# Kernel optimization log

Measured on AMD Instinct MI355X. Metric: run time of the kernel, lower is better.

The kernel has to match this reference:

```python
import jax, jax.numpy as jnp
import numpy as np

B, S, D_IN = 4, 2048, 1024
EMBED, HEADS = 1024, 16
HEAD_DIM = EMBED // HEADS


def setup_inputs() -> dict:
    key = jax.random.key(0)
    k1, k2, k3 = jax.random.split(key, 3)
    x = jax.random.normal(k1, (B, S, D_IN), dtype=jnp.float32)
    # xavier-uniform-ish init scales
    lim_qkv = float(np.sqrt(6.0 / (D_IN + 3 * EMBED)))
    lim_o = float(np.sqrt(6.0 / (EMBED + EMBED)))
    w_qkv = jax.random.uniform(k2, (3 * EMBED, D_IN), minval=-lim_qkv, maxval=lim_qkv, dtype=jnp.float32)
    b_qkv = jnp.zeros((3 * EMBED,), dtype=jnp.float32)
    w_o = jax.random.uniform(k3, (EMBED, EMBED), minval=-lim_o, maxval=lim_o, dtype=jnp.float32)
    b_o = jnp.zeros((EMBED,), dtype=jnp.float32)
    return {"x": x, "w_qkv": w_qkv, "b_qkv": b_qkv, "w_o": w_o, "b_o": b_o}


def reference(x, w_qkv, b_qkv, w_o, b_o):
    b, s, _ = x.shape
    qkv = jnp.einsum('bsi,oi->bso', x, w_qkv) + b_qkv            # (b, s, 3E)
    qkv = qkv.reshape(b, s, HEADS, 3 * HEAD_DIM).transpose(0, 2, 1, 3)  # (b, h, s, 3d)
    q, k, v = jnp.split(qkv, 3, axis=-1)                          # each (b, h, s, d)
    scale = 1.0 / jnp.sqrt(jnp.float32(HEAD_DIM))
    attn = jnp.einsum('bhqd,bhkd->bhqk', q, k) * scale            # (b, h, s, s)
    attn = jax.nn.softmax(attn, axis=-1)
    vals = jnp.einsum('bhqk,bhkd->bhqd', attn, v)                 # (b, h, s, d)
    # NOTE: original torch code reshapes (b,h,s,d) -> (b,s,e) WITHOUT transposing
    # heads back; jnp.reshape reproduces that flattening exactly.
    vals = vals.reshape(b, s, EMBED)
    out = jnp.einsum('bse,oe->bso', vals, w_o) + b_o              # (b, s, E)
    return out
```

## Files before the change

kernel.cpp:

```cpp
#include <hip/hip_runtime.h>
#include <stdint.h>
#include <stddef.h>

#define DEVINL __device__ __forceinline__

typedef unsigned short u16;
typedef unsigned int u32;
typedef __attribute__((ext_vector_type(8))) short short8;
typedef __attribute__((ext_vector_type(4))) float f32x4;
typedef __attribute__((ext_vector_type(4))) u32 u32x4;
typedef __attribute__((ext_vector_type(2))) u32 u32x2;

#define QSCALE 0.18033688011112042f

DEVINL u16 f2bf(float f) {
    u32 u = __builtin_bit_cast(u32, f);
    u32 r = (u + 0x7fffu + ((u >> 16) & 1u)) >> 16;
    return (u16)r;
}

DEVINL void gld_lds16(const void* g, void* l) {
    __builtin_amdgcn_global_load_lds(
        (__attribute__((address_space(1))) u32*)(uintptr_t)g,
        (__attribute__((address_space(3))) u32*)l, 16, 0, 0);
}

DEVINL u32 pack_bf16_trunc(float lo, float hi) {
    return __builtin_amdgcn_perm(__builtin_bit_cast(u32, hi),
                                 __builtin_bit_cast(u32, lo), 0x07060302u);
}

DEVINL void plswap32(u32 &a, u32 &b) {
#if __has_builtin(__builtin_amdgcn_permlane32_swap)
    u32x2 r = __builtin_amdgcn_permlane32_swap(a, b, false, false);
    a = r[0]; b = r[1];
#else
    asm("v_permlane32_swap_b32 %0, %1" : "+v"(a), "+v"(b));
#endif
}
DEVINL void plswap16(u32 &a, u32 &b) {
#if __has_builtin(__builtin_amdgcn_permlane16_swap)
    u32x2 r = __builtin_amdgcn_permlane16_swap(a, b, false, false);
    a = r[0]; b = r[1];
#else
    asm("v_permlane16_swap_b32 %0, %1" : "+v"(a), "+v"(b));
#endif
}

__global__ void prep_inputs(const float* __restrict__ x, const float* __restrict__ wqkv,
                            const float* __restrict__ bqkv, const float* __restrict__ wo,
                            u16* __restrict__ xb, u16* __restrict__ wqb,
                            u16* __restrict__ wob, float* __restrict__ bsc) {
    int blk = blockIdx.x;
    if (blk < 6144) {
        const float* src; u16* dst; int base; bool qscale = false;
        if (blk < 4096)      { src = x;    dst = xb;  base = blk; }
        else if (blk < 5632) { src = wqkv; dst = wqb; base = blk - 4096; qscale = true; }
        else                 { src = wo;   dst = wob; base = blk - 5632; }
        int i = (base * 256 + threadIdx.x) * 8;
        float sc = 1.0f;
        if (qscale) { int row = i >> 10; if ((row % 192) < 64) sc = QSCALE; }
        float4 a = *(const float4*)(src + i);
        float4 c = *(const float4*)(src + i + 4);
        union { u16 s[8]; u32x4 v; } t;
        t.s[0] = f2bf(a.x * sc); t.s[1] = f2bf(a.y * sc); t.s[2] = f2bf(a.z * sc); t.s[3] = f2bf(a.w * sc);
        t.s[4] = f2bf(c.x * sc); t.s[5] = f2bf(c.y * sc); t.s[6] = f2bf(c.z * sc); t.s[7] = f2bf(c.w * sc);
        *(u32x4*)(dst + i) = t.v;
    } else {
        int i = (blk - 6144) * 256 + threadIdx.x;
        float sc = ((i % 192) < 64) ? QSCALE : 1.0f;
        bsc[i] = bqkv[i] * sc;
    }
}

__global__ void gemm_qkv(const u16* __restrict__ A, const u16* __restrict__ Bm,
                         const float* __restrict__ bias, u16* __restrict__ qkvb,
                         u16* __restrict__ vtb) {
    const int K = 1024, N = 3072;
    __shared__ u16 As[128 * 32];
    __shared__ u16 Bs[128 * 32];
    const int tid = threadIdx.x;
    const int lane = tid & 63;
    const int wv = tid >> 6, wr = wv >> 1, wc = wv & 1;
    const int l15 = lane & 15, quad = lane >> 4;
    const int m0 = blockIdx.y * 128, n0 = blockIdx.x * 128;

    f32x4 acc[4][4];
#pragma unroll
    for (int i = 0; i < 4; i++)
#pragma unroll
        for (int j = 0; j < 4; j++) acc[i][j] = (f32x4){0.f, 0.f, 0.f, 0.f};

    const u16* Ab = A + (size_t)m0 * K;
    const u16* Bb = Bm + (size_t)n0 * K;
    const int srow = tid >> 2;
    const int sc8 = (tid & 3) * 8;

    for (int k0 = 0; k0 < K; k0 += 32) {
#pragma unroll
        for (int i = 0; i < 2; i++) {
            int row = i * 64 + srow;
            gld_lds16(Ab + (size_t)row * K + k0 + sc8, (char*)As + (size_t)(i * 256 + tid) * 16);
            gld_lds16(Bb + (size_t)row * K + k0 + sc8, (char*)Bs + (size_t)(i * 256 + tid) * 16);
        }
        __syncthreads();
        short8 af[4], bf8[4];
#pragma unroll
        for (int mi = 0; mi < 4; mi++)
            af[mi] = *(const short8*)(As + (wr * 64 + mi * 16 + l15) * 32 + quad * 8);
#pragma unroll
        for (int ni = 0; ni < 4; ni++)
            bf8[ni] = *(const short8*)(Bs + (wc * 64 + ni * 16 + l15) * 32 + quad * 8);
#pragma unroll
        for (int mi = 0; mi < 4; mi++)
#pragma unroll
            for (int ni = 0; ni < 4; ni++)
                acc[mi][ni] = __builtin_amdgcn_mfma_f32_16x16x32_bf16(af[mi], bf8[ni], acc[mi][ni], 0, 0, 0);
        __syncthreads();
    }

#pragma unroll
    for (int mi = 0; mi < 4; mi++) {
        int row_b = m0 + wr * 64 + mi * 16 + quad * 4;
#pragma unroll
        for (int ni = 0; ni < 4; ni++) {
            int c0 = n0 + wc * 64 + ni * 16;
            int sec0 = c0 % 192;
            float bv = bias[c0 + l15];
            float v0 = acc[mi][ni][0] + bv;
            float v1 = acc[mi][ni][1] + bv;
            float v2 = acc[mi][ni][2] + bv;
            float v3 = acc[mi][ni][3] + bv;
            if (sec0 >= 128) {
                int hh = c0 / 192;
                int b = row_b >> 11;
                int s = row_b & 2047;
                int d = sec0 - 128 + l15;
                u32 lo = (u32)f2bf(v0) | ((u32)f2bf(v1) << 16);
                u32 hi = (u32)f2bf(v2) | ((u32)f2bf(v3) << 16);
                *(u32x2*)(vtb + ((size_t)((b * 16 + hh) * 64 + d)) * 2048 + s) = (u32x2){lo, hi};
            } else {
                int col = c0 + l15;
                qkvb[(size_t)(row_b + 0) * N + col] = f2bf(v0);
                qkvb[(size_t)(row_b + 1) * N + col] = f2bf(v1);
                qkvb[(size_t)(row_b + 2) * N + col] = f2bf(v2);
                qkvb[(size_t)(row_b + 3) * N + col] = f2bf(v3);
            }
        }
    }
}

__global__ void gemm_out(const u16* __restrict__ A, const u16* __restrict__ Bm,
                         const float* __restrict__ bias, float* __restrict__ C) {
    const int K = 1024, N = 1024;
    __shared__ u16 As[128 * 32];
    __shared__ u16 Bs[64 * 32];
    const int tid = threadIdx.x;
    const int lane = tid & 63;
    const int wv = tid >> 6, wr = wv >> 1, wc = wv & 1;
    const int l15 = lane & 15, quad = lane >> 4;
    const int m0 = blockIdx.y * 128, n0 = blockIdx.x * 64;

    f32x4 acc[4][2];
#pragma unroll
    for (int i = 0; i < 4; i++)
#pragma unroll
        for (int j = 0; j < 2; j++) acc[i][j] = (f32x4){0.f, 0.f, 0.f, 0.f};

    const u16* Ab = A + (size_t)m0 * K;
    const u16* Bb = Bm + (size_t)n0 * K;
    const int srow = tid >> 2;
    const int sc8 = (tid & 3) * 8;

    for (int k0 = 0; k0 < K; k0 += 32) {
#pragma unroll
        for (int i = 0; i < 2; i++)
            gld_lds16(Ab + (size_t)(i * 64 + srow) * K + k0 + sc8, (char*)As + (size_t)(i * 256 + tid) * 16);
        gld_lds16(Bb + (size_t)srow * K + k0 + sc8, (char*)Bs + (size_t)tid * 16);
        __syncthreads();
        short8 af[4], bf8[2];
#pragma unroll
        for (int mi = 0; mi < 4; mi++)
            af[mi] = *(const short8*)(As + (wr * 64 + mi * 16 + l15) * 32 + quad * 8);
#pragma unroll
        for (int ni = 0; ni < 2; ni++)
            bf8[ni] = *(const short8*)(Bs + (wc * 32 + ni * 16 + l15) * 32 + quad * 8);
#pragma unroll
        for (int mi = 0; mi < 4; mi++)
#pragma unroll
            for (int ni = 0; ni < 2; ni++)
                acc[mi][ni] = __builtin_amdgcn_mfma_f32_16x16x32_bf16(af[mi], bf8[ni], acc[mi][ni], 0, 0, 0);
        __syncthreads();
    }

#pragma unroll
    for (int mi = 0; mi < 4; mi++) {
        int row_b = m0 + wr * 64 + mi * 16 + quad * 4;
#pragma unroll
        for (int ni = 0; ni < 2; ni++) {
            int col = n0 + wc * 32 + ni * 16 + l15;
            float bv = bias[col];
#pragma unroll
            for (int r = 0; r < 4; r++)
                C[(size_t)(row_b + r) * N + col] = acc[mi][ni][r] + bv;
        }
    }
}

__launch_bounds__(256, 4)
__global__ void flash_attn(const u16* __restrict__ qkv, const u16* __restrict__ vt,
                           u16* __restrict__ vals2) {
    __shared__ u16 Ks[2][64 * 64];
    __shared__ u16 Vts[2][64 * 64];

    const int tid = threadIdx.x;
    const int lane = tid & 63, wv = tid >> 6;
    const int l15 = lane & 15, quad = lane >> 4;
    const int e7 = (l15 & 7) * 8;
    const int id = blockIdx.x;
    const int m = id >> 3;
    const int bh = ((id & 7) << 3) + (m >> 4);
    const int s0 = (m & 15) << 7;
    const int b = bh >> 4, h = bh & 15;

    short8 qf[2][2];
    const u16* qbase = qkv + (size_t)(b * 2048 + s0 + wv * 32) * 3072 + h * 192;
#pragma unroll
    for (int qi = 0; qi < 2; qi++)
#pragma unroll
        for (int ks = 0; ks < 2; ks++)
            qf[qi][ks] = *(const short8*)(qbase + (size_t)(qi * 16 + l15) * 3072 + ks * 32 + quad * 8);

    f32x4 o_acc[2][4];
    f32x4 sum_acc[2];
#pragma unroll
    for (int qi = 0; qi < 2; qi++) {
        sum_acc[qi] = (f32x4){0.f, 0.f, 0.f, 0.f};
#pragma unroll
        for (int nd = 0; nd < 4; nd++) o_acc[qi][nd] = (f32x4){0.f, 0.f, 0.f, 0.f};
    }

    const u16* kg = qkv + (size_t)(b * 2048) * 3072 + h * 192 + 64;
    const u16* vg = vt + (size_t)bh * 64 * 2048;

    const int lrow = lane >> 3;
    const int lgr  = (lane & 7) ^ lrow;
    const int r0   = wv * 8 + lrow;

    const short8 ones = (short8){0x3F80, 0x3F80, 0x3F80, 0x3F80, 0x3F80, 0x3F80, 0x3F80, 0x3F80};

#pragma unroll
    for (int j = 0; j < 2; j++) {
        int row = j * 32 + r0;
        gld_lds16(kg + (size_t)row * 3072 + lgr * 8, (char*)&Ks[0][0] + (size_t)(j * 256 + tid) * 16);
        gld_lds16(vg + (size_t)row * 2048 + lgr * 8, (char*)&Vts[0][0] + (size_t)(j * 256 + tid) * 16);
    }
    __syncthreads();

    int cur = 0;
    for (int kb = 0; kb < 2048; kb += 64) {
        if (kb + 64 < 2048) {
            int nb = cur ^ 1;
#pragma unroll
            for (int j = 0; j < 2; j++) {
                int row = j * 32 + r0;
                gld_lds16(kg + (size_t)(kb + 64 + row) * 3072 + lgr * 8,
                          (char*)&Ks[nb][0] + (size_t)(j * 256 + tid) * 16);
                gld_lds16(vg + (size_t)row * 2048 + kb + 64 + lgr * 8,
                          (char*)&Vts[nb][0] + (size_t)(j * 256 + tid) * 16);
            }
        }

        f32x4 s_acc[4][2];
#pragma unroll
        for (int ki = 0; ki < 4; ki++)
#pragma unroll
            for (int qi = 0; qi < 2; qi++) s_acc[ki][qi] = (f32x4){0.f, 0.f, 0.f, 0.f};
        __builtin_amdgcn_s_setprio(1);
#pragma unroll
        for (int ki = 0; ki < 4; ki++) {
#pragma unroll
            for (int ks = 0; ks < 2; ks++) {
                short8 kf = *(const short8*)(&Ks[cur][0] + (ki * 16 + l15) * 64 + ((ks * 32 + quad * 8) ^ e7));
#pragma unroll
                for (int qi = 0; qi < 2; qi++)
                    s_acc[ki][qi] = __builtin_amdgcn_mfma_f32_16x16x32_bf16(kf, qf[qi][ks], s_acc[ki][qi], 0, 0, 0);
            }
        }
        __builtin_amdgcn_s_setprio(0);

        short8 ap[2][2];
#pragma unroll
        for (int c = 0; c < 2; c++)
#pragma unroll
            for (int qi = 0; qi < 2; qi++) {
                u32 w0 = pack_bf16_trunc(__builtin_amdgcn_exp2f(s_acc[2 * c][qi][0]),
                                         __builtin_amdgcn_exp2f(s_acc[2 * c][qi][1]));
                u32 w1 = pack_bf16_trunc(__builtin_amdgcn_exp2f(s_acc[2 * c][qi][2]),
                                         __builtin_amdgcn_exp2f(s_acc[2 * c][qi][3]));
                u32 w2 = pack_bf16_trunc(__builtin_amdgcn_exp2f(s_acc[2 * c + 1][qi][0]),
                                         __builtin_amdgcn_exp2f(s_acc[2 * c + 1][qi][1]));
                u32 w3 = pack_bf16_trunc(__builtin_amdgcn_exp2f(s_acc[2 * c + 1][qi][2]),
                                         __builtin_amdgcn_exp2f(s_acc[2 * c + 1][qi][3]));
                plswap32(w0, w2);
                plswap32(w1, w3);
                plswap16(w0, w2);
                plswap16(w1, w3);
                u32x4 wf = (u32x4){w0, w1, w2, w3};
                ap[qi][c] = __builtin_bit_cast(short8, wf);
            }

#pragma unroll
        for (int c = 0; c < 2; c++) {
#pragma unroll
            for (int qi = 0; qi < 2; qi++)
                sum_acc[qi] = __builtin_amdgcn_mfma_f32_16x16x32_bf16(ap[qi][c], ones, sum_acc[qi], 0, 0, 0);
            __builtin_amdgcn_s_setprio(1);
#pragma unroll
            for (int nd = 0; nd < 4; nd++) {
                short8 bv = *(const short8*)(&Vts[cur][0] + (nd * 16 + l15) * 64 + ((c * 32 + quad * 8) ^ e7));
#pragma unroll
                for (int qi = 0; qi < 2; qi++)
                    o_acc[qi][nd] = __builtin_amdgcn_mfma_f32_16x16x32_bf16(ap[qi][c], bv, o_acc[qi][nd], 0, 0, 0);
            }
            __builtin_amdgcn_s_setprio(0);
        }

        __syncthreads();
        cur ^= 1;
    }

#pragma unroll
    for (int qi = 0; qi < 2; qi++) {
        f32x4 inv;
#pragma unroll
        for (int r = 0; r < 4; r++) inv[r] = 1.0f / sum_acc[qi][r];
#pragma unroll
        for (int nd = 0; nd < 4; nd++) {
            int d = nd * 16 + l15;
#pragma unroll
            for (int r = 0; r < 4; r++) {
                int s = s0 + wv * 32 + qi * 16 + quad * 4 + r;
                size_t row2 = (size_t)(b * 2048 + h * 128 + (s >> 4));
                int col2 = ((s & 15) << 6) + d;
                vals2[row2 * 1024 + col2] = f2bf(o_acc[qi][nd][r] * inv[r]);
            }
        }
    }
}

extern "C" void kernel_launch(void* const* d_in, const int* in_sizes, int n_in,
                              void* d_out, int out_size, void* d_ws, size_t ws_size,
                              hipStream_t stream) {
    (void)in_sizes; (void)n_in; (void)out_size; (void)ws_size;
    const float* x      = (const float*)d_in[0];
    const float* w_qkv  = (const float*)d_in[1];
    const float* b_qkv  = (const float*)d_in[2];
    const float* w_o    = (const float*)d_in[3];
    const float* b_o    = (const float*)d_in[4];
    float* out = (float*)d_out;

    char* ws = (char*)d_ws;
    u16* xb   = (u16*)(ws);
    u16* wqb  = (u16*)(ws + 16777216);
    u16* wob  = (u16*)(ws + 23068672);
    u16* qkvb = (u16*)(ws + 25165824);
    u16* vtb  = (u16*)(ws + 75497472);
    u16* v2b  = (u16*)(ws + 92274688);
    float* bsc = (float*)(ws + 92274688);

    prep_inputs<<<6156, 256, 0, stream>>>(x, w_qkv, b_qkv, w_o, xb, wqb, wob, bsc);

    gemm_qkv<<<dim3(24, 64), 256, 0, stream>>>(xb, wqb, bsc, qkvb, vtb);

    flash_attn<<<1024, 256, 0, stream>>>(qkvb, vtb, v2b);

    gemm_out<<<dim3(16, 64), 256, 0, stream>>>(v2b, wob, b_o, out);
}
```

Measured before the change: 270.5 us.

## Remap GEMM blocks per XCD and store K/V tiles fragment-ordered in LDS

Both GEMMs move to a 1D grid whose block index is decoded so that each XCD (selected by id & 7) works on a contiguous band of M rows, improving L2 reuse of A tiles within an XCD. In flash attention, the K and V^T tiles are written to LDS already arranged in MFMA fragment order, so each lane reads one contiguous 16-byte slot at lane*16 plus a constant offset. This replaces the XOR-swizzled row addressing and cuts the address arithmetic per LDS read. The global loads into LDS now gather 16-row fragments, which changes their coalescing pattern and could make them less efficient.

```diff
diff --git a/kernel.cpp b/kernel.cpp
--- a/kernel.cpp
+++ b/kernel.cpp
@@ -83,7 +83,10 @@
     const int lane = tid & 63;
     const int wv = tid >> 6, wr = wv >> 1, wc = wv & 1;
     const int l15 = lane & 15, quad = lane >> 4;
-    const int m0 = blockIdx.y * 128, n0 = blockIdx.x * 128;
+    const int id = blockIdx.x;
+    const int xcd = id & 7, rr = id >> 3;
+    const int m0 = ((xcd << 3) + rr / 24) * 128;
+    const int n0 = (rr % 24) * 128;
 
     f32x4 acc[4][4];
 #pragma unroll
@@ -159,7 +162,10 @@
     const int lane = tid & 63;
     const int wv = tid >> 6, wr = wv >> 1, wc = wv & 1;
     const int l15 = lane & 15, quad = lane >> 4;
-    const int m0 = blockIdx.y * 128, n0 = blockIdx.x * 64;
+    const int id = blockIdx.x;
+    const int xcd = id & 7, rr = id >> 3;
+    const int m0 = ((xcd << 3) + (rr >> 4)) * 128;
+    const int n0 = (rr & 15) * 64;
 
     f32x4 acc[4][2];
 #pragma unroll
@@ -216,7 +222,6 @@
     const int tid = threadIdx.x;
     const int lane = tid & 63, wv = tid >> 6;
     const int l15 = lane & 15, quad = lane >> 4;
-    const int e7 = (l15 & 7) * 8;
     const int id = blockIdx.x;
     const int m = id >> 3;
     const int bh = ((id & 7) << 3) + (m >> 4);
@@ -243,17 +248,20 @@
     const u16* kg = qkv + (size_t)(b * 2048) * 3072 + h * 192 + 64;
     const u16* vg = vt + (size_t)bh * 64 * 2048;
 
-    const int lrow = lane >> 3;
-    const int lgr  = (lane & 7) ^ lrow;
-    const int r0   = wv * 8 + lrow;
+    size_t ksrc[2], vsrc[2];
+#pragma unroll
+    for (int j = 0; j < 2; j++) {
+        int f = j * 4 + wv, fi = f >> 1, fs = f & 1;
+        ksrc[j] = (size_t)(fi * 16 + l15) * 3072 + fs * 32 + quad * 8;
+        vsrc[j] = (size_t)(fi * 16 + l15) * 2048 + fs * 32 + quad * 8;
+    }
 
     const short8 ones = (short8){0x3F80, 0x3F80, 0x3F80, 0x3F80, 0x3F80, 0x3F80, 0x3F80, 0x3F80};
 
 #pragma unroll
     for (int j = 0; j < 2; j++) {
-        int row = j * 32 + r0;
-        gld_lds16(kg + (size_t)row * 3072 + lgr * 8, (char*)&Ks[0][0] + (size_t)(j * 256 + tid) * 16);
-        gld_lds16(vg + (size_t)row * 2048 + lgr * 8, (char*)&Vts[0][0] + (size_t)(j * 256 + tid) * 16);
+        gld_lds16(kg + ksrc[j], (char*)&Ks[0][0] + (size_t)(j * 256 + tid) * 16);
+        gld_lds16(vg + vsrc[j], (char*)&Vts[0][0] + (size_t)(j * 256 + tid) * 16);
     }
     __syncthreads();
 
@@ -263,13 +271,15 @@
             int nb = cur ^ 1;
 #pragma unroll
             for (int j = 0; j < 2; j++) {
-                int row = j * 32 + r0;
-                gld_lds16(kg + (size_t)(kb + 64 + row) * 3072 + lgr * 8,
+                gld_lds16(kg + (size_t)(kb + 64) * 3072 + ksrc[j],
                           (char*)&Ks[nb][0] + (size_t)(j * 256 + tid) * 16);
-                gld_lds16(vg + (size_t)row * 2048 + kb + 64 + lgr * 8,
+                gld_lds16(vg + (kb + 64) + vsrc[j],
                           (char*)&Vts[nb][0] + (size_t)(j * 256 + tid) * 16);
             }
         }
+
+        const char* kbase = (const char*)&Ks[cur][0] + lane * 16;
+        const char* vbase = (const char*)&Vts[cur][0] + lane * 16;
 
         f32x4 s_acc[4][2];
 #pragma unroll
@@ -281,7 +291,7 @@
         for (int ki = 0; ki < 4; ki++) {
 #pragma unroll
             for (int ks = 0; ks < 2; ks++) {
-                short8 kf = *(const short8*)(&Ks[cur][0] + (ki * 16 + l15) * 64 + ((ks * 32 + quad * 8) ^ e7));
+                short8 kf = *(const short8*)(kbase + (ki * 2 + ks) * 1024);
 #pragma unroll
                 for (int qi = 0; qi < 2; qi++)
                     s_acc[ki][qi] = __builtin_amdgcn_mfma_f32_16x16x32_bf16(kf, qf[qi][ks], s_acc[ki][qi], 0, 0, 0);
@@ -318,7 +328,7 @@
             __builtin_amdgcn_s_setprio(1);
 #pragma unroll
             for (int nd = 0; nd < 4; nd++) {
-                short8 bv = *(const short8*)(&Vts[cur][0] + (nd * 16 + l15) * 64 + ((c * 32 + quad * 8) ^ e7));
+                short8 bv = *(const short8*)(vbase + (nd * 2 + c) * 1024);
 #pragma unroll
                 for (int qi = 0; qi < 2; qi++)
                     o_acc[qi][nd] = __builtin_amdgcn_mfma_f32_16x16x32_bf16(ap[qi][c], bv, o_acc[qi][nd], 0, 0, 0);
@@ -371,9 +381,9 @@
 
     prep_inputs<<<6156, 256, 0, stream>>>(x, w_qkv, b_qkv, w_o, xb, wqb, wob, bsc);
 
-    gemm_qkv<<<dim3(24, 64), 256, 0, stream>>>(xb, wqb, bsc, qkvb, vtb);
+    gemm_qkv<<<1536, 256, 0, stream>>>(xb, wqb, bsc, qkvb, vtb);
 
     flash_attn<<<1024, 256, 0, stream>>>(qkvb, vtb, v2b);
 
-    gemm_out<<<dim3(16, 64), 256, 0, stream>>>(v2b, wob, b_o, out);
-}
+    gemm_out<<<1024, 256, 0, stream>>>(v2b, wob, b_o, out);
+}
```

Measured after the change: 269.5 us. Within noise of the previous version (-0.4%).
